# Kernel optimization log

Hardware: AMD Instinct MI355X
Metric: run time of the kernel (lower is better)

Reference implementation:

```python
import jax, jax.numpy as jnp
import numpy as np

N_TYPES = 10000   # len(fs.inodes)
HID = 256         # fs.size
BATCH = 32
SEQ = 1024


def _build_tree(rng):
    # random recursive tree: parent[i] uniform in [0, i), root parent = -1
    parent = np.full(N_TYPES, -1, np.int64)
    parent[1:] = (rng.random(N_TYPES - 1) * np.arange(1, N_TYPES)).astype(np.int64)
    # depth (number of nodes on root path incl. self)
    depth = np.ones(N_TYPES, np.int64)
    for i in range(1, N_TYPES):
        depth[i] = depth[parent[i]] + 1
    D = int(depth.max())
    # ancestor table: anc[n, d] = d-th ancestor of n (anc[n,0]=n), -1 padding
    anc = np.full((N_TYPES, D), -1, np.int32)
    anc[:, 0] = np.arange(N_TYPES)
    cur = parent.copy()
    for d in range(1, D):
        anc[:, d] = cur
        cur = np.where(cur >= 0, parent[np.maximum(cur, 0)], -1)
    return anc


def setup_inputs() -> dict:
    key = jax.random.key(0)
    ks = jax.random.split(key, 8)
    rng = np.random.default_rng(0)
    anc = jnp.asarray(_build_tree(rng))  # [N, D] int32
    k = 1.0 / np.sqrt(HID)
    inp = {
        "event_seqs": jax.random.randint(ks[0], (BATCH, SEQ), 0, N_TYPES),
        "anc": anc,
        "weight": jax.random.uniform(ks[1], (N_TYPES,), jnp.float32, -0.1, 0.1),
        "emb": jax.random.normal(ks[2], (N_TYPES, HID), jnp.float32),
        "W_ih": jax.random.uniform(ks[3], (4 * HID, HID), jnp.float32, -k, k),
        "W_hh": jax.random.uniform(ks[4], (4 * HID, HID), jnp.float32, -k, k),
        "b_ih": jax.random.uniform(ks[5], (4 * HID,), jnp.float32, -k, k),
        "b_hh": jax.random.uniform(ks[6], (4 * HID,), jnp.float32, -k, k),
    }
    return inp


def _path_table(anc, weight, emb):
    # path[n] = sum_d (prod_{j<d} weight[anc[n,j]]) * emb[anc[n,d]], over valid ancestors
    valid = anc >= 0                                  # [N, D]
    anc_safe = jnp.where(valid, anc, 0)
    w = jnp.where(valid, weight[anc_safe], 1.0)       # [N, D]
    cumw = jnp.cumprod(w, axis=1)
    cumw = jnp.concatenate([jnp.ones_like(cumw[:, :1]), cumw[:, :-1]], axis=1)
    cumw = jnp.where(valid, cumw, 0.0)
    e = emb[anc_safe]                                 # [N, D, H]
    return jnp.einsum("nd,ndh->nh", cumw, e)          # [N, H]


def _lstm(emb_seq, W_ih, W_hh, b_ih, b_hh):
    # emb_seq: [T, B, H]; torch LSTM gate order i, f, g, o
    H = W_hh.shape[1]
    B = emb_seq.shape[1]
    x_proj = jnp.einsum("tbh,gh->tbg", emb_seq, W_ih) + b_ih + b_hh  # [T, B, 4H]

    def step(carry, x_t):
        h, c = carry
        gates = x_t + h @ W_hh.T
        i, f, g, o = jnp.split(gates, 4, axis=-1)
        i, f, o = jax.nn.sigmoid(i), jax.nn.sigmoid(f), jax.nn.sigmoid(o)
        g = jnp.tanh(g)
        c = f * c + i * g
        h = o * jnp.tanh(c)
        return (h, c), h

    h0 = jnp.zeros((B, H), emb_seq.dtype)
    (hn, cn), out = jax.lax.scan(step, (h0, h0), x_proj)
    return out, hn, cn


def reference(event_seqs, anc, weight, emb, W_ih, W_hh, b_ih, b_hh):
    path = _path_table(anc, weight, emb)       # [N, H]
    emb_seq = path[event_seqs.T]               # [T, B, H] (torch transposes to seq-first)
    out, hn, cn = _lstm(emb_seq, W_ih, W_hh, b_ih, b_hh)
    return out
```

## Files before the change

kernel.cpp:

```cpp
#include <hip/hip_runtime.h>

typedef unsigned int uint;
typedef unsigned long long u64;
typedef unsigned short ushort;
typedef _Float16 f16;
typedef _Float16 f16x2 __attribute__((ext_vector_type(2)));
typedef _Float16 f16x8 __attribute__((ext_vector_type(8)));
typedef float f32x4 __attribute__((ext_vector_type(4)));

#define N_TYPES 10000
#define HID 256
#define G4 1024
#define BATCH 32
#define SEQ 1024

__global__ void k_path(const int* __restrict__ anc, const float* __restrict__ weight,
                       const float* __restrict__ emb, int D, f16* __restrict__ path) {
  int n = blockIdx.x;
  int h = threadIdx.x;
  float acc = 0.f, cw = 1.f;
  for (int d = 0; d < D; ++d) {
    int a = anc[n * D + d];
    if (a < 0) break;
    acc += cw * emb[a * HID + h];
    cw *= weight[a];
  }
  path[n * HID + h] = (f16)acc;
}

__global__ void k_conv(const float* __restrict__ wih, const float* __restrict__ whh,
                       const float* __restrict__ bih, const float* __restrict__ bhh,
                       f16* __restrict__ wih_h, uint* __restrict__ whh_t,
                       float* __restrict__ bias) {
  int i = blockIdx.x * 256 + threadIdx.x;
  wih_h[i] = (f16)wih[i];
  if (i < G4 * 128) {
    int row = i >> 7, p = i & 127;
    f16x2 v;
    v.x = (f16)whh[row * HID + 2 * p];
    v.y = (f16)whh[row * HID + 2 * p + 1];
    whh_t[p * G4 + row] = __builtin_bit_cast(uint, v);
  }
  if (i < G4) bias[i] = bih[i] + bhh[i];
}

#define BM 128
#define BN 128
#define BK 64
#define LPAD 72
__global__ __launch_bounds__(256) void k_gemm(const f16* __restrict__ A,
                                              const f16* __restrict__ Bw,
                                              const float* __restrict__ bias,
                                              f16* __restrict__ C) {
  __shared__ f16 sA[BM][LPAD];
  __shared__ f16 sB[BN][LPAD];
  int m0 = blockIdx.x * BM, n0 = blockIdx.y * BN;
  int tid = threadIdx.x;
  int wid = tid >> 6, lane = tid & 63;
  int wm = wid & 1, wn = wid >> 1;
  f32x4 acc[4][4] = {};
  for (int k0 = 0; k0 < 256; k0 += BK) {
    __syncthreads();
    int r = tid >> 3, kc = (tid & 7) * 8;
    for (int i = 0; i < 4; ++i) {
      int row = r + 32 * i;
      int gm = m0 + row;
      uint4 va = make_uint4(0u, 0u, 0u, 0u);
      if (gm < N_TYPES) va = *(const uint4*)&A[gm * 256 + k0 + kc];
      *(uint4*)&sA[row][kc] = va;
      uint4 vb = *(const uint4*)&Bw[(n0 + row) * 256 + k0 + kc];
      *(uint4*)&sB[row][kc] = vb;
    }
    __syncthreads();
#pragma unroll
    for (int ks = 0; ks < 2; ++ks) {
      f16x8 af[4], bf[4];
      int kk = ks * 32 + (lane >> 4) * 8;
#pragma unroll
      for (int mt = 0; mt < 4; ++mt)
        af[mt] = *(const f16x8*)&sA[wm * 64 + mt * 16 + (lane & 15)][kk];
#pragma unroll
      for (int nt = 0; nt < 4; ++nt)
        bf[nt] = *(const f16x8*)&sB[wn * 64 + nt * 16 + (lane & 15)][kk];
#pragma unroll
      for (int mt = 0; mt < 4; ++mt)
#pragma unroll
        for (int nt = 0; nt < 4; ++nt)
          acc[mt][nt] = __builtin_amdgcn_mfma_f32_16x16x32_f16(af[mt], bf[nt], acc[mt][nt], 0, 0, 0);
    }
  }
#pragma unroll
  for (int mt = 0; mt < 4; ++mt)
#pragma unroll
    for (int nt = 0; nt < 4; ++nt)
#pragma unroll
      for (int qq = 0; qq < 4; ++qq) {
        int row = m0 + wm * 64 + mt * 16 + (lane >> 4) * 4 + qq;
        int col = n0 + wn * 64 + nt * 16 + (lane & 15);
        int dim = col & 255, g = col >> 8;
        if (row < N_TYPES)
          C[row * G4 + dim * 4 + g] = (f16)(acc[mt][nt][qq] + bias[col]);
      }
}

__device__ __forceinline__ float dot2(uint wp, uint hp, float acc) {
#if __has_builtin(__builtin_amdgcn_fdot2)
  return __builtin_amdgcn_fdot2(__builtin_bit_cast(f16x2, wp),
                                __builtin_bit_cast(f16x2, hp), acc, false);
#else
  f16x2 a = __builtin_bit_cast(f16x2, wp);
  f16x2 b = __builtin_bit_cast(f16x2, hp);
  return acc + (float)a.x * (float)b.x + (float)a.y * (float)b.y;
#endif
}

__device__ __forceinline__ float sigm(float v) { return 1.f / (1.f + __expf(-v)); }
__device__ __forceinline__ float tanh_(float v) { return 1.f - 2.f / (__expf(2.f * v) + 1.f); }
__device__ __forceinline__ float f16u(ushort u) { return (float)__builtin_bit_cast(f16, u); }

__global__ __launch_bounds__(512)
void k_lstm(const int* __restrict__ evs,
            const f16* __restrict__ proj,
            const uint* __restrict__ whh_t,
            u64* hglob,
            float* __restrict__ out) {
  int bid = blockIdx.x;
  int b = bid & 31, q = bid >> 5;
  int t = threadIdx.x;
  int v = t >> 6, l = t & 63;
  int kq = v >> 1;
  int rid = (v & 1) * 64 + l;
  int rowg = (rid >> 5) * 256 + q * 32 + (rid & 31);

  __shared__ uint4 wlds[8 * 512];
  __shared__ float pl[2][128][4];

  {
    const uint* wb = whh_t + (kq * 32) * G4 + rowg;
#pragma unroll
    for (int i4 = 0; i4 < 8; ++i4) {
      uint4 wv;
      wv.x = wb[(4 * i4 + 0) * G4];
      wv.y = wb[(4 * i4 + 1) * G4];
      wv.z = wb[(4 * i4 + 2) * G4];
      wv.w = wb[(4 * i4 + 3) * G4];
      wlds[i4 * 512 + t] = wv;
    }
  }
  __syncthreads();

  u64* hb = hglob + b * 256;
  const int* ev = evs + b * SEQ;

  float x0 = 0.f, x1 = 0.f, x2 = 0.f, x3 = 0.f;
  if (t < 32) {
    ushort4 xv = *(const ushort4*)(proj + (long)ev[0] * G4 + (q * 32 + t) * 4);
    x0 = f16u(xv.x); x1 = f16u(xv.y); x2 = f16u(xv.z); x3 = f16u(xv.w);
  }

  float c = 0.f;

  for (int step = 0; step < SEQ; ++step) {
    int h0 = 0;
    if (step > 0 && l < 32) {
      const u64* src = hb + ((step - 1) & 1) * 128 + kq * 32 + l;
      u64 val;
      do {
        val = __hip_atomic_load(src, __ATOMIC_RELAXED, __HIP_MEMORY_SCOPE_AGENT);
      } while ((uint)(val >> 32) != (uint)step);
      h0 = (int)(uint)val;
    }

    float a0 = 0.f, a1 = 0.f, a2 = 0.f, a3 = 0.f;
#pragma unroll
    for (int i4 = 0; i4 < 8; ++i4) {
      uint4 wv = wlds[i4 * 512 + t];
      a0 = dot2(wv.x, (uint)__builtin_amdgcn_readlane(h0, 4 * i4 + 0), a0);
      a1 = dot2(wv.y, (uint)__builtin_amdgcn_readlane(h0, 4 * i4 + 1), a1);
      a2 = dot2(wv.z, (uint)__builtin_amdgcn_readlane(h0, 4 * i4 + 2), a2);
      a3 = dot2(wv.w, (uint)__builtin_amdgcn_readlane(h0, 4 * i4 + 3), a3);
    }
    pl[step & 1][rid][kq] = (a0 + a1) + (a2 + a3);

    float n0 = 0.f, n1 = 0.f, n2 = 0.f, n3 = 0.f;
    if (t < 32 && step + 1 < SEQ) {
      ushort4 xv = *(const ushort4*)(proj + (long)ev[step + 1] * G4 + (q * 32 + t) * 4);
      n0 = f16u(xv.x); n1 = f16u(xv.y); n2 = f16u(xv.z); n3 = f16u(xv.w);
    }

    __syncthreads();

    if (t < 32) {
      f32x4 p0 = *(const f32x4*)&pl[step & 1][t][0];
      f32x4 p1 = *(const f32x4*)&pl[step & 1][32 + t][0];
      f32x4 p2 = *(const f32x4*)&pl[step & 1][64 + t][0];
      f32x4 p3 = *(const f32x4*)&pl[step & 1][96 + t][0];
      float s0 = (p0[0] + p0[1]) + (p0[2] + p0[3]) + x0;
      float s1 = (p1[0] + p1[1]) + (p1[2] + p1[3]) + x1;
      float s2 = (p2[0] + p2[1]) + (p2[2] + p2[3]) + x2;
      float s3 = (p3[0] + p3[1]) + (p3[2] + p3[3]) + x3;
      float iv = sigm(s0), fv = sigm(s1), gv = tanh_(s2), ov = sigm(s3);
      c = fv * c + iv * gv;
      float hval = ov * tanh_(c);
      out[(step * BATCH + b) * HID + q * 32 + t] = hval;
      float hA = __shfl(hval, 2 * (t & 15));
      float hB = __shfl(hval, 2 * (t & 15) + 1);
      if (t < 16) {
        f16x2 pk; pk.x = (f16)hA; pk.y = (f16)hB;
        u64 val = (u64)__builtin_bit_cast(uint, pk) | ((u64)(uint)(step + 1) << 32);
        __hip_atomic_store(hb + (step & 1) * 128 + q * 16 + t, val,
                           __ATOMIC_RELAXED, __HIP_MEMORY_SCOPE_AGENT);
      }
    }
    x0 = n0; x1 = n1; x2 = n2; x3 = n3;
  }
}

extern "C" void kernel_launch(void* const* d_in, const int* in_sizes, int n_in,
                              void* d_out, int out_size, void* d_ws, size_t ws_size,
                              hipStream_t stream) {
  (void)n_in; (void)out_size; (void)ws_size;
  const int* evs = (const int*)d_in[0];
  const int* anc = (const int*)d_in[1];
  const float* weight = (const float*)d_in[2];
  const float* emb = (const float*)d_in[3];
  const float* wih = (const float*)d_in[4];
  const float* whh = (const float*)d_in[5];
  const float* bih = (const float*)d_in[6];
  const float* bhh = (const float*)d_in[7];
  int D = in_sizes[1] / N_TYPES;

  char* ws = (char*)d_ws;
  f16* path = (f16*)(ws);
  f16* wih_h = (f16*)(ws + 5242880);
  uint* whh_t = (uint*)(ws + 5767168);
  float* bias = (float*)(ws + 6291456);
  f16* proj = (f16*)(ws + 6295552);
  u64* hglob = (u64*)(ws + 26775552);
  float* out = (float*)d_out;

  k_conv<<<1024, 256, 0, stream>>>(wih, whh, bih, bhh, wih_h, whh_t, bias);
  k_path<<<N_TYPES, 256, 0, stream>>>(anc, weight, emb, D, path);
  k_gemm<<<dim3(79, 8), 256, 0, stream>>>(path, wih_h, bias, proj);
  hipMemsetAsync(hglob, 0, 32 * 2 * 128 * 8, stream);
  k_lstm<<<256, 512, 0, stream>>>(evs, proj, whh_t, hglob, out);
}
```

Baseline: 1.815 ms.

## Detect same-XCD batch groups and use workgroup-scope CAS polling for h exchange

Each LSTM block reads its hardware XCC id and publishes it in a small map. It then checks whether all 8 blocks sharing a batch row landed on the same XCD. If they did, the per-step hidden-state handoff uses workgroup-scope compare-exchange polling and plain volatile stores, which avoids device-scope coherence traffic. Otherwise it falls back to agent-scope atomics. The partial-sum LDS layout is transposed to [kq][rid], and the output store is moved after the h publish so the cross-block signal goes out sooner. Relying on workgroup scope for cross-CU visibility is a subtle memory-model risk, and blockIdx-to-XCD placement usually spreads blocks round-robin, so the fast path may rarely trigger.

```diff
diff --git a/kernel.cpp b/kernel.cpp
--- a/kernel.cpp
+++ b/kernel.cpp
@@ -123,6 +123,7 @@
             const f16* __restrict__ proj,
             const uint* __restrict__ whh_t,
             u64* hglob,
+            uint* xcd_map,
             float* __restrict__ out) {
   int bid = blockIdx.x;
   int b = bid & 31, q = bid >> 5;
@@ -133,7 +134,7 @@
   int rowg = (rid >> 5) * 256 + q * 32 + (rid & 31);
 
   __shared__ uint4 wlds[8 * 512];
-  __shared__ float pl[2][128][4];
+  __shared__ float pl[2][4][128];
 
   {
     const uint* wb = whh_t + (kq * 32) * G4 + rowg;
@@ -147,6 +148,21 @@
       wlds[i4 * 512 + t] = wv;
     }
   }
+
+  uint xid;
+  asm volatile("s_getreg_b32 %0, hwreg(HW_REG_XCC_ID)" : "=s"(xid));
+  if (t == 0)
+    __hip_atomic_store(&xcd_map[bid], xid + 1u, __ATOMIC_RELAXED, __HIP_MEMORY_SCOPE_AGENT);
+  uint e = 0;
+  if (l < 8) {
+    const uint* mp = &xcd_map[l * 32 + b];
+    do {
+      e = __hip_atomic_load(mp, __ATOMIC_RELAXED, __HIP_MEMORY_SCOPE_AGENT);
+    } while (e == 0);
+  }
+  uint e0 = (uint)__builtin_amdgcn_readfirstlane((int)e);
+  bool fast = __all((l >= 8) || (e == e0));
+
   __syncthreads();
 
   u64* hb = hglob + b * 256;
@@ -163,11 +179,20 @@
   for (int step = 0; step < SEQ; ++step) {
     int h0 = 0;
     if (step > 0 && l < 32) {
-      const u64* src = hb + ((step - 1) & 1) * 128 + kq * 32 + l;
+      u64* src = hb + ((step - 1) & 1) * 128 + kq * 32 + l;
       u64 val;
-      do {
-        val = __hip_atomic_load(src, __ATOMIC_RELAXED, __HIP_MEMORY_SCOPE_AGENT);
-      } while ((uint)(val >> 32) != (uint)step);
+      if (fast) {
+        do {
+          u64 exp = 0ull;
+          __hip_atomic_compare_exchange_strong(src, &exp, 0ull,
+              __ATOMIC_RELAXED, __ATOMIC_RELAXED, __HIP_MEMORY_SCOPE_WORKGROUP);
+          val = exp;
+        } while ((uint)(val >> 32) != (uint)step);
+      } else {
+        do {
+          val = __hip_atomic_load(src, __ATOMIC_RELAXED, __HIP_MEMORY_SCOPE_AGENT);
+        } while ((uint)(val >> 32) != (uint)step);
+      }
       h0 = (int)(uint)val;
     }
 
@@ -180,7 +205,7 @@
       a2 = dot2(wv.z, (uint)__builtin_amdgcn_readlane(h0, 4 * i4 + 2), a2);
       a3 = dot2(wv.w, (uint)__builtin_amdgcn_readlane(h0, 4 * i4 + 3), a3);
     }
-    pl[step & 1][rid][kq] = (a0 + a1) + (a2 + a3);
+    pl[step & 1][kq][rid] = (a0 + a1) + (a2 + a3);
 
     float n0 = 0.f, n1 = 0.f, n2 = 0.f, n3 = 0.f;
     if (t < 32 && step + 1 < SEQ) {
@@ -191,26 +216,27 @@
     __syncthreads();
 
     if (t < 32) {
-      f32x4 p0 = *(const f32x4*)&pl[step & 1][t][0];
-      f32x4 p1 = *(const f32x4*)&pl[step & 1][32 + t][0];
-      f32x4 p2 = *(const f32x4*)&pl[step & 1][64 + t][0];
-      f32x4 p3 = *(const f32x4*)&pl[step & 1][96 + t][0];
-      float s0 = (p0[0] + p0[1]) + (p0[2] + p0[3]) + x0;
-      float s1 = (p1[0] + p1[1]) + (p1[2] + p1[3]) + x1;
-      float s2 = (p2[0] + p2[1]) + (p2[2] + p2[3]) + x2;
-      float s3 = (p3[0] + p3[1]) + (p3[2] + p3[3]) + x3;
+      const float (*pp)[128] = pl[step & 1];
+      float s0 = (pp[0][t]      + pp[1][t])      + (pp[2][t]      + pp[3][t])      + x0;
+      float s1 = (pp[0][32 + t] + pp[1][32 + t]) + (pp[2][32 + t] + pp[3][32 + t]) + x1;
+      float s2 = (pp[0][64 + t] + pp[1][64 + t]) + (pp[2][64 + t] + pp[3][64 + t]) + x2;
+      float s3 = (pp[0][96 + t] + pp[1][96 + t]) + (pp[2][96 + t] + pp[3][96 + t]) + x3;
       float iv = sigm(s0), fv = sigm(s1), gv = tanh_(s2), ov = sigm(s3);
       c = fv * c + iv * gv;
       float hval = ov * tanh_(c);
-      out[(step * BATCH + b) * HID + q * 32 + t] = hval;
       float hA = __shfl(hval, 2 * (t & 15));
       float hB = __shfl(hval, 2 * (t & 15) + 1);
       if (t < 16) {
         f16x2 pk; pk.x = (f16)hA; pk.y = (f16)hB;
         u64 val = (u64)__builtin_bit_cast(uint, pk) | ((u64)(uint)(step + 1) << 32);
-        __hip_atomic_store(hb + (step & 1) * 128 + q * 16 + t, val,
-                           __ATOMIC_RELAXED, __HIP_MEMORY_SCOPE_AGENT);
+        u64* dst = hb + (step & 1) * 128 + q * 16 + t;
+        if (fast) {
+          *(volatile u64*)dst = val;
+        } else {
+          __hip_atomic_store(dst, val, __ATOMIC_RELAXED, __HIP_MEMORY_SCOPE_AGENT);
+        }
       }
+      out[(step * BATCH + b) * HID + q * 32 + t] = hval;
     }
     x0 = n0; x1 = n1; x2 = n2; x3 = n3;
   }
@@ -237,11 +263,12 @@
   float* bias = (float*)(ws + 6291456);
   f16* proj = (f16*)(ws + 6295552);
   u64* hglob = (u64*)(ws + 26775552);
+  uint* xcd_map = (uint*)(ws + 26841088);
   float* out = (float*)d_out;
 
   k_conv<<<1024, 256, 0, stream>>>(wih, whh, bih, bhh, wih_h, whh_t, bias);
   k_path<<<N_TYPES, 256, 0, stream>>>(anc, weight, emb, D, path);
   k_gemm<<<dim3(79, 8), 256, 0, stream>>>(path, wih_h, bias, proj);
-  hipMemsetAsync(hglob, 0, 32 * 2 * 128 * 8, stream);
-  k_lstm<<<256, 512, 0, stream>>>(evs, proj, whh_t, hglob, out);
-}
+  hipMemsetAsync(hglob, 0, 65536 + 1024, stream);
+  k_lstm<<<256, 512, 0, stream>>>(evs, proj, whh_t, hglob, xcd_map, out);
+}
```

After: 4.219 ms. 2.32x slower.
